# Optimization experiments

Hardware: AMD Instinct MI355X
Metric: run time of the kernel (lower is better)

## Reference

```python
import jax, jax.numpy as jnp
import numpy as np

B, T, C, H = 8, 1024, 1024, 16
D = C // H
EPS = 1e-5

def _ln(x, g, b):
    mu = jnp.mean(x, axis=-1, keepdims=True)
    var = jnp.var(x, axis=-1, keepdims=True)
    return (x - mu) * jax.lax.rsqrt(var + EPS) * g + b

def _build_mask(cond_mask, cond_len, token_len):
    # Vectorized form of the per-batch Python-loop mask in the torch module.
    counts = jnp.sum(cond_mask, axis=-1)            # [B] number of valid cond tokens
    rows = jnp.arange(T)
    cols = jnp.arange(T)
    # all rows may attend to the first counts[i] (cond) columns
    m_cond = cols[None, None, :] < counts[:, None, None]          # [B,1,T]
    m_cond = jnp.broadcast_to(m_cond, (B, T, T))
    # block-causal tiled pattern on rows/cols >= cond_len:
    # value = (col - cond_len) % token_len <= (row - cond_len) % token_len
    pattern = ((cols[None, :] - cond_len) % token_len) <= ((rows[:, None] - cond_len) % token_len)
    m_block = (rows[:, None] >= cond_len) & (cols[None, :] >= cond_len) & pattern  # [T,T]
    # cols >= cond_len: overwritten by block pattern (rows < cond_len stay 0 there)
    mask = jnp.where(cols[None, None, :] < cond_len, m_cond, m_block[None, :, :])
    return mask[:, None, :, :]                      # [B,1,T,T] bool

def _attn(x, Wq, bq, Wk, bk, Wv, bv, Wp, bp, cond_mask, cond_len, token_len):
    q = (x @ Wq + bq).reshape(B, T, H, D).transpose(0, 2, 1, 3)  # [B,H,T,D]
    k = (x @ Wk + bk).reshape(B, T, H, D).transpose(0, 2, 1, 3)
    v = (x @ Wv + bv).reshape(B, T, H, D).transpose(0, 2, 1, 3)
    att = jnp.einsum('bhqd,bhkd->bhqk', q, k) * (1.0 / np.sqrt(D))
    mask = _build_mask(cond_mask, cond_len, token_len)
    att = jnp.where(mask, att, -jnp.inf)
    att = jax.nn.softmax(att, axis=-1)
    y = jnp.einsum('bhqk,bhkd->bhqd', att, v)
    y = y.transpose(0, 2, 1, 3).reshape(B, T, C)
    return y @ Wp + bp

def setup_inputs() -> dict:
    key = jax.random.key(0)
    ks = jax.random.split(key, 16)
    cond_len, token_len = 256, 768
    s = 1.0 / np.sqrt(C)
    counts = jax.random.randint(ks[0], (B,), 1, cond_len + 1)
    cond_mask = (jnp.arange(T)[None, :] < counts[:, None]).astype(jnp.int32)
    return {
        'x': jax.random.normal(ks[1], (B, T, C), jnp.float32),
        'ln1_g': jnp.ones((C,), jnp.float32), 'ln1_b': jnp.zeros((C,), jnp.float32),
        'Wq': jax.random.normal(ks[2], (C, C), jnp.float32) * s, 'bq': jnp.zeros((C,), jnp.float32),
        'Wk': jax.random.normal(ks[3], (C, C), jnp.float32) * s, 'bk': jnp.zeros((C,), jnp.float32),
        'Wv': jax.random.normal(ks[4], (C, C), jnp.float32) * s, 'bv': jnp.zeros((C,), jnp.float32),
        'Wp': jax.random.normal(ks[5], (C, C), jnp.float32) * s, 'bp': jnp.zeros((C,), jnp.float32),
        'ln2_g': jnp.ones((C,), jnp.float32), 'ln2_b': jnp.zeros((C,), jnp.float32),
        'W1': jax.random.normal(ks[6], (C, 4 * C), jnp.float32) * s, 'b1': jnp.zeros((4 * C,), jnp.float32),
        'W2': jax.random.normal(ks[7], (4 * C, C), jnp.float32) * (0.5 * s), 'b2': jnp.zeros((C,), jnp.float32),
        'cond_mask': cond_mask,
        'cond_len': cond_len,
        'token_len': token_len,
    }

def reference(x, ln1_g, ln1_b, Wq, bq, Wk, bk, Wv, bv, Wp, bp, ln2_g, ln2_b, W1, b1, W2, b2, cond_mask, cond_len, token_len):
    x = x + _attn(_ln(x, ln1_g, ln1_b), Wq, bq, Wk, bk, Wv, bv, Wp, bp, cond_mask, cond_len, token_len)
    h = _ln(x, ln2_g, ln2_b)
    x = x + (jax.nn.gelu(h @ W1 + b1, approximate=False) @ W2 + b2)
    return x
```

## Files before the change

### kernel.cpp

```cpp
#include <hip/hip_runtime.h>
#include <hip/hip_bf16.h>
#include <cstdint>
#include <cstddef>

typedef __attribute__((ext_vector_type(8))) short short8;
typedef __attribute__((ext_vector_type(4))) float f32x4;
typedef __attribute__((ext_vector_type(4))) unsigned short us4;

#define MFMA_BF16(a, b, c) __builtin_amdgcn_mfma_f32_16x16x32_bf16((a), (b), (c), 0, 0, 0)
#define VMCNT(n) asm volatile("s_waitcnt vmcnt(" #n ")" ::: "memory")

__device__ __forceinline__ unsigned short f2bf(float f) {
  unsigned int u = __float_as_uint(f);
  u += 0x7FFFu + ((u >> 16) & 1u);
  return (unsigned short)(u >> 16);
}

__device__ __forceinline__ float gelu_fast(float v) {
  const float u = v * (0.79788456f + 0.03567741f * v * v);
  const float e = exp2f(u * 2.88539008f);
  return v - v * __builtin_amdgcn_rcpf(e + 1.0f);
}

typedef const void __attribute__((address_space(1)))* as1_cvp;
typedef void __attribute__((address_space(3)))* as3_vp;
__device__ __forceinline__ void gll16(const short* g, short* l) {
#if defined(__HIP_DEVICE_COMPILE__)
  __builtin_amdgcn_global_load_lds((as1_cvp)g, (as3_vp)l, 16, 0, 0);
#else
  (void)g; (void)l;
#endif
}

__global__ void count_kernel(const int* __restrict__ cm, int* __restrict__ counts) {
  __shared__ int sd[256];
  const int b = blockIdx.x, t = threadIdx.x;
  int s = 0;
  for (int i = t; i < 1024; i += 256) s += cm[b * 1024 + i];
  sd[t] = s; __syncthreads();
  for (int k = 128; k > 0; k >>= 1) { if (t < k) sd[t] += sd[t + k]; __syncthreads(); }
  if (t == 0) counts[b] = sd[0];
}

__global__ void pack_bias_kernel(const float* __restrict__ bq, const float* __restrict__ bk,
                                 const float* __restrict__ bv, float* __restrict__ dst) {
  int i = blockIdx.x * 256 + threadIdx.x;
  dst[i] = (i < 1024) ? bq[i] : (i < 2048 ? bk[i - 1024] : bv[i - 2048]);
}

__global__ void transpose_kernel(const float* __restrict__ src, unsigned short* __restrict__ dst,
                                 int R, int C) {
  __shared__ float tile[32][33];
  const int c0 = blockIdx.x * 32, r0 = blockIdx.y * 32;
  const int tx = threadIdx.x, ty = threadIdx.y;
  #pragma unroll
  for (int i = ty; i < 32; i += 8)
    tile[i][tx] = src[(size_t)(r0 + i) * C + (c0 + tx)];
  __syncthreads();
  #pragma unroll
  for (int i = ty; i < 32; i += 8)
    dst[(size_t)(c0 + i) * R + (r0 + tx)] = f2bf(tile[tx][i]);
}

__global__ void vtrans_kernel(const short* __restrict__ qkv, short* __restrict__ vtr) {
  __shared__ short tile[32][33];
  const int bh = blockIdx.z;
  const int t0 = blockIdx.x * 32, d0 = blockIdx.y * 32;
  const int b = bh >> 4, h = bh & 15;
  const int tx = threadIdx.x, ty = threadIdx.y;
  const short* src = qkv + (size_t)b * 1024 * 3072 + 2048 + h * 64;
  #pragma unroll
  for (int i = ty; i < 32; i += 8)
    tile[i][tx] = src[(size_t)(t0 + i) * 3072 + d0 + tx];
  __syncthreads();
  short* dst = vtr + (size_t)bh * 65536;
  #pragma unroll
  for (int i = ty; i < 32; i += 8)
    dst[(d0 + i) * 1024 + t0 + tx] = tile[tx][i];
}

__global__ __launch_bounds__(64) void kvpack_kernel(
    const short* __restrict__ qkv, const short* __restrict__ vtr,
    short* __restrict__ kp, short* __restrict__ vp) {
  const int blk = blockIdx.x;
  const int bh = blk >> 5, ti = blk & 31;
  const int b = bh >> 4, h = bh & 15;
  const int l = threadIdx.x & 63;
  const int lq = l & 15, g = l >> 4;
  const int kv0 = ti * 32;
  const int permrow = 8 * (lq >> 2) + (lq & 3);
  const short* ka = qkv + (size_t)b * 1024 * 3072 + h * 64
                    + (size_t)(kv0 + permrow) * 3072 + 1024 + 8 * g;
  short* kd = kp + (size_t)blk * 2048 + l * 8;
  *(short8*)(kd)        = *(const short8*)ka;
  *(short8*)(kd + 512)  = *(const short8*)(ka + 32);
  *(short8*)(kd + 1024) = *(const short8*)(ka + 4 * 3072);
  *(short8*)(kd + 1536) = *(const short8*)(ka + 4 * 3072 + 32);
  const short* vb = vtr + (size_t)bh * 65536;
  short* vd = vp + (size_t)blk * 2048 + l * 8;
  #pragma unroll
  for (int dc = 0; dc < 4; ++dc)
    *(short8*)(vd + dc * 512) =
        *(const short8*)(vb + (16 * dc + lq) * 1024 + kv0 + 8 * g);
}

__global__ __launch_bounds__(256) void ln_kernel(const float* __restrict__ in,
                                                 const float* __restrict__ gw,
                                                 const float* __restrict__ bw,
                                                 unsigned short* __restrict__ out) {
  const int row = blockIdx.x, t = threadIdx.x;
  const float4 v = ((const float4*)(in + (size_t)row * 1024))[t];
  float s = v.x + v.y + v.z + v.w;
  float ss = v.x * v.x + v.y * v.y + v.z * v.z + v.w * v.w;
  #pragma unroll
  for (int o = 32; o >= 1; o >>= 1) { s += __shfl_down(s, o, 64); ss += __shfl_down(ss, o, 64); }
  __shared__ float red[8];
  if ((t & 63) == 0) { red[t >> 6] = s; red[4 + (t >> 6)] = ss; }
  __syncthreads();
  const float S  = red[0] + red[1] + red[2] + red[3];
  const float SS = red[4] + red[5] + red[6] + red[7];
  const float mu = S * (1.0f / 1024.0f);
  const float var = SS * (1.0f / 1024.0f) - mu * mu;
  const float rs = rsqrtf(var + 1e-5f);
  const int c = t * 4;
  const float4 g4 = ((const float4*)gw)[t];
  const float4 b4 = ((const float4*)bw)[t];
  us4 o4;
  o4[0] = f2bf((v.x - mu) * rs * g4.x + b4.x);
  o4[1] = f2bf((v.y - mu) * rs * g4.y + b4.y);
  o4[2] = f2bf((v.z - mu) * rs * g4.z + b4.z);
  o4[3] = f2bf((v.w - mu) * rs * g4.w + b4.w);
  *(us4*)(out + (size_t)row * 1024 + c) = o4;
}

template <int EPI>
__global__ __launch_bounds__(256, 2) void gemm128_kernel(
    const short* __restrict__ A, const short* __restrict__ BT,
    const float* __restrict__ bias, int N, int K, int gm,
    unsigned short* __restrict__ outb, float* __restrict__ outf,
    const float* __restrict__ res) {
  __shared__ alignas(16) short lds[36864];
  const int t = threadIdx.x;
  const int l = t & 63, w = t >> 6;
  const int lq = l & 15, g = l >> 4;
  const int wc = w;
  const int cpx = (int)gridDim.x >> 3;
  const int wid = ((int)blockIdx.x & 7) * cpx + ((int)blockIdx.x >> 3);
  const int bm = (wid % gm) * 128, bn = (wid / gm) * 256;
  const int NT = K >> 5;

  const int csw = ((t & 3) ^ ((t >> 3) & 3)) * 8;
  const int sr = t >> 2;

  const f32x4 z4 = {0.f, 0.f, 0.f, 0.f};
  f32x4 acc[8][4];
  #pragma unroll
  for (int i = 0; i < 8; i++)
    #pragma unroll
    for (int j = 0; j < 4; j++) acc[i][j] = z4;

  auto stageA = [&](int buf, int k0) {
    const short* src = A + (size_t)(bm + sr) * K + k0 + csw;
    short* dst = lds + buf * 12288 + t * 8;
    gll16(src, dst);
    gll16(src + (size_t)64 * K, dst + 2048);
  };
  auto stageB = [&](int buf, int k0) {
    const short* src = BT + (size_t)(bn + sr) * K + k0 + csw;
    short* dst = lds + buf * 12288 + 4096 + t * 8;
    gll16(src, dst);
    gll16(src + (size_t)64 * K,  dst + 2048);
    gll16(src + (size_t)128 * K, dst + 4096);
    gll16(src + (size_t)192 * K, dst + 6144);
  };
  const int swu = (g ^ ((lq >> 1) & 3)) * 8;
  auto rdA = [&](int buf, int mi) {
    const int ra = mi * 16 + lq;
    return *(const short8*)(lds + buf * 12288 + ra * 32 + swu);
  };
  auto rdB = [&](int buf, int ni) {
    const int rb = wc * 64 + ni * 16 + lq;
    return *(const short8*)(lds + buf * 12288 + 4096 + rb * 32 + swu);
  };

  stageA(0, 0);  stageB(0, 0);
  stageA(1, 32); stageB(1, 32);
  VMCNT(6);
  __builtin_amdgcn_s_barrier();

  int cur = 0;
  for (int v = 0; v < NT; ++v) {
    const int nx1 = (cur == 2) ? 0 : cur + 1;
    const int nx2 = (nx1 == 2) ? 0 : nx1 + 1;
    short8 a[8], b[4];
    #pragma unroll
    for (int mi = 0; mi < 8; ++mi) a[mi] = rdA(cur, mi);
    #pragma unroll
    for (int ni = 0; ni < 4; ++ni) b[ni] = rdB(cur, ni);
    if (v + 2 < NT) {
      stageA(nx2, (v + 2) * 32); stageB(nx2, (v + 2) * 32);
      VMCNT(6);
    } else {
      VMCNT(0);
    }
    __builtin_amdgcn_s_barrier();
    __builtin_amdgcn_s_setprio(1);
    #pragma unroll
    for (int mi = 0; mi < 8; ++mi)
      #pragma unroll
      for (int ni = 0; ni < 4; ++ni)
        acc[mi][ni] = MFMA_BF16(a[mi], b[ni], acc[mi][ni]);
    __builtin_amdgcn_s_setprio(0);
    cur = nx1;
  }

  if (EPI == 2) {
    #pragma unroll
    for (int mi = 0; mi < 8; ++mi) {
      #pragma unroll
      for (int ni = 0; ni < 4; ++ni) {
        const int col = bn + wc * 64 + ni * 16 + lq;
        const float bv = bias[col];
        #pragma unroll
        for (int r = 0; r < 4; ++r) {
          const int row = bm + mi * 16 + 4 * g + r;
          const size_t idx = (size_t)row * N + col;
          outf[idx] = acc[mi][ni][r] + bv + res[idx];
        }
      }
    }
    return;
  }

  __syncthreads();
  const float qscale = (EPI == 3 && bn < 1024) ? 0.125f * 1.44269504088896f : 1.0f;
  unsigned short* eb = (unsigned short*)lds;
  #pragma unroll
  for (int mi = 0; mi < 8; ++mi) {
    #pragma unroll
    for (int ni = 0; ni < 4; ++ni) {
      const int col = wc * 64 + ni * 16 + lq;
      const float bv = bias[bn + col];
      #pragma unroll
      for (int r = 0; r < 4; ++r) {
        const int row = mi * 16 + 4 * g + r;
        float vv = acc[mi][ni][r] + bv;
        if (EPI == 1) vv = gelu_fast(vv);
        if (EPI == 3) vv *= qscale;
        eb[row * 256 + col] = f2bf(vv);
      }
    }
  }
  __syncthreads();
  #pragma unroll
  for (int it = 0; it < 16; ++it) {
    const int unit = it * 256 + t;
    const int row = unit >> 5, c8 = unit & 31;
    const short8 vv = *(const short8*)(lds + unit * 8);
    *(short8*)((short*)outb + (size_t)(bm + row) * N + bn + c8 * 8) = vv;
  }
}

__global__ __launch_bounds__(256) void attn_kernel(
    const short* __restrict__ qkv, const short* __restrict__ kp,
    const short* __restrict__ vp, unsigned short* __restrict__ y,
    const int* __restrict__ counts) {
  const int blk = blockIdx.x;
  const int slot = blk >> 3;
  const int pb = slot & 7;
  const int bh = ((slot >> 3) << 3) | (blk & 7);
  const int b = bh >> 4, h = bh & 15;
  const int w = threadIdx.x >> 6, l = threadIdx.x & 63;
  const int p = pb + 8 * w;
  const int lq = l & 15, g = l >> 4;
  const int qb0 = p * 16, qb1 = (63 - p) * 16;
  const int count = counts[b];

  const short* base  = qkv + (size_t)b * 1024 * 3072 + h * 64;
  const short* kbase = kp + (size_t)bh * 65536 + l * 8;
  const short* vbase = vp + (size_t)bh * 65536 + l * 8;

  short8 qf[2][2];
  {
    const short* qr0 = base + (size_t)(qb0 + lq) * 3072 + 8 * g;
    const short* qr1 = base + (size_t)(qb1 + lq) * 3072 + 8 * g;
    qf[0][0] = *(const short8*)qr0; qf[0][1] = *(const short8*)(qr0 + 32);
    qf[1][0] = *(const short8*)qr1; qf[1][1] = *(const short8*)(qr1 + 32);
  }

  const f32x4 z4 = {0.f, 0.f, 0.f, 0.f};
  f32x4 oacc[2][4];
  #pragma unroll
  for (int grp = 0; grp < 2; ++grp)
    #pragma unroll
    for (int dc = 0; dc < 4; ++dc) oacc[grp][dc] = z4;
  float mrun[2] = {-1e30f, -1e30f};
  float lrun[2] = {0.f, 0.f};
  const int ncond = min((count + 31) >> 5, 8);
  const int ncausal = (qb1 + 16 - 256 + 31) >> 5;
  const int nt = ncond + ncausal;
  auto kv_of = [&](int i) { return i < ncond ? i * 32 : 256 + (i - ncond) * 32; };

  auto loadt = [&](int kv0, short8 (&kr)[4], short8 (&vr)[4]) {
    const short* kpp = kbase + (size_t)(kv0 >> 5) * 2048;
    kr[0] = *(const short8*)kpp;
    kr[1] = *(const short8*)(kpp + 512);
    kr[2] = *(const short8*)(kpp + 1024);
    kr[3] = *(const short8*)(kpp + 1536);
    const short* vpp = vbase + (size_t)(kv0 >> 5) * 2048;
    #pragma unroll
    for (int dc = 0; dc < 4; ++dc)
      vr[dc] = *(const short8*)(vpp + dc * 512);
  };

  auto compute = [&](int i, const short8 (&kr)[4], const short8 (&vr)[4]) {
    const int kv0 = kv_of(i);
    const bool isCond = (i < ncond);
    #pragma unroll
    for (int grp = 0; grp < 2; ++grp) {
      const int qb = grp ? qb1 : qb0;
      if (!isCond && kv0 >= qb + 16) continue;
      const bool needMask = isCond ? (kv0 + 32 > count) : (kv0 + 31 > qb);
      f32x4 sA = z4, sB = z4;
      __builtin_amdgcn_s_setprio(1);
      sA = MFMA_BF16(kr[0], qf[grp][0], sA);
      sA = MFMA_BF16(kr[1], qf[grp][1], sA);
      sB = MFMA_BF16(kr[2], qf[grp][0], sB);
      sB = MFMA_BF16(kr[3], qf[grp][1], sB);
      __builtin_amdgcn_s_setprio(0);
      const int q = qb + lq;
      float mx = -1e30f;
      if (needMask) {
        #pragma unroll
        for (int r = 0; r < 4; ++r) {
          const int colA = kv0 + 8 * g + r, colB = colA + 4;
          const bool okA = isCond ? (colA < count) : (colA <= q);
          const bool okB = isCond ? (colB < count) : (colB <= q);
          const float vA = okA ? sA[r] : -1e30f;
          const float vB = okB ? sB[r] : -1e30f;
          sA[r] = vA; sB[r] = vB;
          mx = fmaxf(fmaxf(vA, vB), mx);
        }
      } else {
        #pragma unroll
        for (int r = 0; r < 4; ++r)
          mx = fmaxf(fmaxf(sA[r], sB[r]), mx);
      }
      mx = fmaxf(mx, __shfl_xor(mx, 16, 64));
      mx = fmaxf(mx, __shfl_xor(mx, 32, 64));
      float m = mrun[grp];
      if (!__all(mx <= m + 8.0f)) {
        const float mn = fmaxf(m, mx);
        const float sf = exp2f(m - mn);
        lrun[grp] *= sf;
        #pragma unroll
        for (int dc = 0; dc < 4; ++dc)
          #pragma unroll
          for (int r = 0; r < 4; ++r) oacc[grp][dc][r] *= sf;
        mrun[grp] = mn; m = mn;
      }
      float ps = 0.f;
      #pragma unroll
      for (int r = 0; r < 4; ++r) {
        const float aa = exp2f(sA[r] - m);
        const float c2 = exp2f(sB[r] - m);
        sA[r] = aa; sB[r] = c2; ps += aa + c2;
      }
      lrun[grp] += ps;
      union { short8 s8; __hip_bfloat162 h2[4]; } pu;
      pu.h2[0] = __float22bfloat162_rn(float2{sA[0], sA[1]});
      pu.h2[1] = __float22bfloat162_rn(float2{sA[2], sA[3]});
      pu.h2[2] = __float22bfloat162_rn(float2{sB[0], sB[1]});
      pu.h2[3] = __float22bfloat162_rn(float2{sB[2], sB[3]});
      __builtin_amdgcn_s_setprio(1);
      #pragma unroll
      for (int dc = 0; dc < 4; ++dc)
        oacc[grp][dc] = MFMA_BF16(vr[dc], pu.s8, oacc[grp][dc]);
      __builtin_amdgcn_s_setprio(0);
    }
  };

  short8 kb0[4], vb0[4], kb1[4], vb1[4];
  loadt(kv_of(0), kb0, vb0);
  for (int i = 0; i < nt; i += 2) {
    if (i + 1 < nt) loadt(kv_of(i + 1), kb1, vb1);
    compute(i, kb0, vb0);
    if (i + 1 >= nt) break;
    if (i + 2 < nt) loadt(kv_of(i + 2), kb0, vb0);
    compute(i + 1, kb1, vb1);
  }

  #pragma unroll
  for (int grp = 0; grp < 2; ++grp) {
    float ls = lrun[grp];
    ls += __shfl_xor(ls, 16, 64);
    ls += __shfl_xor(ls, 32, 64);
    const float inv = 1.0f / ls;
    const int qb = grp ? qb1 : qb0;
    unsigned short* yr = y + (size_t)(b * 1024 + qb + lq) * 1024 + h * 64;
    #pragma unroll
    for (int dc = 0; dc < 4; ++dc)
      #pragma unroll
      for (int r = 0; r < 4; ++r)
        yr[16 * dc + 4 * g + r] = f2bf(oacc[grp][dc][r] * inv);
  }
}

extern "C" void kernel_launch(void* const* d_in, const int* in_sizes, int n_in,
                              void* d_out, int out_size, void* d_ws, size_t ws_size,
                              hipStream_t stream) {
  (void)in_sizes; (void)n_in; (void)out_size; (void)ws_size;
  const float* x     = (const float*)d_in[0];
  const float* ln1_g = (const float*)d_in[1];
  const float* ln1_b = (const float*)d_in[2];
  const float* Wq    = (const float*)d_in[3];
  const float* bq    = (const float*)d_in[4];
  const float* Wk    = (const float*)d_in[5];
  const float* bk    = (const float*)d_in[6];
  const float* Wv    = (const float*)d_in[7];
  const float* bv    = (const float*)d_in[8];
  const float* Wp    = (const float*)d_in[9];
  const float* bp    = (const float*)d_in[10];
  const float* ln2_g = (const float*)d_in[11];
  const float* ln2_b = (const float*)d_in[12];
  const float* W1    = (const float*)d_in[13];
  const float* b1    = (const float*)d_in[14];
  const float* W2    = (const float*)d_in[15];
  const float* b2    = (const float*)d_in[16];
  const int* cond_mask = (const int*)d_in[17];

  char* ws = (char*)d_ws;
  const size_t MB = 1u << 20;
  short* xn    = (short*)(ws + 0);
  short* kpack = (short*)(ws + 0);
  short* qkv   = (short*)(ws + 16 * MB);
  short* act   = (short*)(ws + 0);
  unsigned short* yb = (unsigned short*)(ws + 64 * MB);
  short* vtr   = (short*)(ws + 80 * MB);
  float* x1    = (float*)(ws + 80 * MB);
  short* vpack = (short*)(ws + 112 * MB);
  short* hb    = (short*)(ws + 112 * MB);
  short* wqkvT = (short*)(ws + 128 * MB);
  short* wpT   = (short*)(ws + 134 * MB);
  short* w1T   = (short*)(ws + 136 * MB);
  short* w2T   = (short*)(ws + 144 * MB);
  float* bqkv  = (float*)(ws + 152 * MB);
  int* counts  = (int*)(ws + 152 * MB + 16384);

  const dim3 tb(32, 8);
  count_kernel<<<8, 256, 0, stream>>>(cond_mask, counts);
  pack_bias_kernel<<<12, 256, 0, stream>>>(bq, bk, bv, bqkv);
  transpose_kernel<<<dim3(32, 32), tb, 0, stream>>>(Wq, (unsigned short*)wqkvT, 1024, 1024);
  transpose_kernel<<<dim3(32, 32), tb, 0, stream>>>(Wk, (unsigned short*)(wqkvT + 1024 * 1024), 1024, 1024);
  transpose_kernel<<<dim3(32, 32), tb, 0, stream>>>(Wv, (unsigned short*)(wqkvT + 2 * 1024 * 1024), 1024, 1024);
  transpose_kernel<<<dim3(32, 32), tb, 0, stream>>>(Wp, (unsigned short*)wpT, 1024, 1024);
  transpose_kernel<<<dim3(128, 32), tb, 0, stream>>>(W1, (unsigned short*)w1T, 1024, 4096);
  transpose_kernel<<<dim3(32, 128), tb, 0, stream>>>(W2, (unsigned short*)w2T, 4096, 1024);
  ln_kernel<<<8192, 256, 0, stream>>>(x, ln1_g, ln1_b, (unsigned short*)xn);

  gemm128_kernel<3><<<768, 256, 0, stream>>>(xn, wqkvT, bqkv, 3072, 1024, 64,
                                             (unsigned short*)qkv, nullptr, nullptr);
  vtrans_kernel<<<dim3(32, 2, 128), tb, 0, stream>>>(qkv, vtr);
  kvpack_kernel<<<4096, 64, 0, stream>>>(qkv, vtr, kpack, vpack);
  attn_kernel<<<1024, 256, 0, stream>>>(qkv, kpack, vpack, yb, counts);
  gemm128_kernel<2><<<256, 256, 0, stream>>>((const short*)yb, wpT, bp, 1024, 1024, 64,
                                             nullptr, x1, x);
  ln_kernel<<<8192, 256, 0, stream>>>(x1, ln2_g, ln2_b, (unsigned short*)hb);
  gemm128_kernel<1><<<1024, 256, 0, stream>>>(hb, w1T, b1, 4096, 1024, 64,
                                              (unsigned short*)act, nullptr, nullptr);
  gemm128_kernel<2><<<256, 256, 0, stream>>>(act, w2T, b2, 1024, 4096, 64,
                                             nullptr, (float*)d_out, x1);
}
```

Measured before the change: 409.6 us.

## Split-K the FC2 GEMM into two slices with a separate reduction kernel

The final 4096-deep GEMM, previously launched with only 256 workgroups, now runs as two K-halves of 2048. This doubles the grid to 512 blocks so more of the CUs are busy. Each slice writes bf16 partial results, and a new elementwise kernel sums them and adds the bias and the residual in fp32. In exchange the kernel adds partial-buffer traffic and an extra launch, and the partials are rounded to bf16 before summation, which loses some precision.

```diff
diff --git a/kernel.cpp b/kernel.cpp
--- a/kernel.cpp
+++ b/kernel.cpp
@@ -133,19 +133,41 @@
   *(us4*)(out + (size_t)row * 1024 + c) = o4;
 }
 
+__global__ __launch_bounds__(256) void red_kernel(
+    const unsigned short* __restrict__ p0, const unsigned short* __restrict__ p1,
+    const float* __restrict__ bias, const float* __restrict__ res,
+    float* __restrict__ out) {
+  const int i = (blockIdx.x * 256 + threadIdx.x) * 4;
+  const us4 a = *(const us4*)(p0 + i);
+  const us4 b = *(const us4*)(p1 + i);
+  const float4 r = *(const float4*)(res + i);
+  const float4 bv = *(const float4*)(bias + (i & 1023));
+  float4 o;
+  o.x = __uint_as_float((unsigned)a[0] << 16) + __uint_as_float((unsigned)b[0] << 16) + bv.x + r.x;
+  o.y = __uint_as_float((unsigned)a[1] << 16) + __uint_as_float((unsigned)b[1] << 16) + bv.y + r.y;
+  o.z = __uint_as_float((unsigned)a[2] << 16) + __uint_as_float((unsigned)b[2] << 16) + bv.z + r.z;
+  o.w = __uint_as_float((unsigned)a[3] << 16) + __uint_as_float((unsigned)b[3] << 16) + bv.w + r.w;
+  *(float4*)(out + i) = o;
+}
+
 template <int EPI>
 __global__ __launch_bounds__(256, 2) void gemm128_kernel(
     const short* __restrict__ A, const short* __restrict__ BT,
-    const float* __restrict__ bias, int N, int K, int gm,
-    unsigned short* __restrict__ outb, float* __restrict__ outf,
-    const float* __restrict__ res) {
+    const float* __restrict__ bias, int N, int K, int kstr, int gm, int skoff,
+    unsigned short* __restrict__ outb, unsigned short* __restrict__ outb2,
+    float* __restrict__ outf, const float* __restrict__ res) {
   __shared__ alignas(16) short lds[36864];
   const int t = threadIdx.x;
   const int l = t & 63, w = t >> 6;
   const int lq = l & 15, g = l >> 4;
   const int wc = w;
   const int cpx = (int)gridDim.x >> 3;
-  const int wid = ((int)blockIdx.x & 7) * cpx + ((int)blockIdx.x >> 3);
+  int wid = ((int)blockIdx.x & 7) * cpx + ((int)blockIdx.x >> 3);
+  int slice = 0;
+  if (EPI == 4) { slice = wid >> 8; wid &= 255; }
+  const short* Ap = A + (size_t)slice * skoff;
+  const short* Bp = BT + (size_t)slice * skoff;
+  unsigned short* outp = (EPI == 4 && slice) ? outb2 : outb;
   const int bm = (wid % gm) * 128, bn = (wid / gm) * 256;
   const int NT = K >> 5;
 
@@ -160,18 +182,18 @@
     for (int j = 0; j < 4; j++) acc[i][j] = z4;
 
   auto stageA = [&](int buf, int k0) {
-    const short* src = A + (size_t)(bm + sr) * K + k0 + csw;
+    const short* src = Ap + (size_t)(bm + sr) * kstr + k0 + csw;
     short* dst = lds + buf * 12288 + t * 8;
     gll16(src, dst);
-    gll16(src + (size_t)64 * K, dst + 2048);
+    gll16(src + (size_t)64 * kstr, dst + 2048);
   };
   auto stageB = [&](int buf, int k0) {
-    const short* src = BT + (size_t)(bn + sr) * K + k0 + csw;
+    const short* src = Bp + (size_t)(bn + sr) * kstr + k0 + csw;
     short* dst = lds + buf * 12288 + 4096 + t * 8;
     gll16(src, dst);
-    gll16(src + (size_t)64 * K,  dst + 2048);
-    gll16(src + (size_t)128 * K, dst + 4096);
-    gll16(src + (size_t)192 * K, dst + 6144);
+    gll16(src + (size_t)64 * kstr,  dst + 2048);
+    gll16(src + (size_t)128 * kstr, dst + 4096);
+    gll16(src + (size_t)192 * kstr, dst + 6144);
   };
   const int swu = (g ^ ((lq >> 1) & 3)) * 8;
   auto rdA = [&](int buf, int mi) {
@@ -240,7 +262,7 @@
     #pragma unroll
     for (int ni = 0; ni < 4; ++ni) {
       const int col = wc * 64 + ni * 16 + lq;
-      const float bv = bias[bn + col];
+      const float bv = (EPI == 4) ? 0.f : bias[bn + col];
       #pragma unroll
       for (int r = 0; r < 4; ++r) {
         const int row = mi * 16 + 4 * g + r;
@@ -257,7 +279,7 @@
     const int unit = it * 256 + t;
     const int row = unit >> 5, c8 = unit & 31;
     const short8 vv = *(const short8*)(lds + unit * 8);
-    *(short8*)((short*)outb + (size_t)(bm + row) * N + bn + c8 * 8) = vv;
+    *(short8*)((short*)outp + (size_t)(bm + row) * N + bn + c8 * 8) = vv;
   }
 }
 
@@ -436,10 +458,12 @@
   short* qkv   = (short*)(ws + 16 * MB);
   short* act   = (short*)(ws + 0);
   unsigned short* yb = (unsigned short*)(ws + 64 * MB);
+  unsigned short* part0 = (unsigned short*)(ws + 64 * MB);
   short* vtr   = (short*)(ws + 80 * MB);
   float* x1    = (float*)(ws + 80 * MB);
   short* vpack = (short*)(ws + 112 * MB);
   short* hb    = (short*)(ws + 112 * MB);
+  unsigned short* part1 = (unsigned short*)(ws + 112 * MB);
   short* wqkvT = (short*)(ws + 128 * MB);
   short* wpT   = (short*)(ws + 134 * MB);
   short* w1T   = (short*)(ws + 136 * MB);
@@ -458,16 +482,17 @@
   transpose_kernel<<<dim3(32, 128), tb, 0, stream>>>(W2, (unsigned short*)w2T, 4096, 1024);
   ln_kernel<<<8192, 256, 0, stream>>>(x, ln1_g, ln1_b, (unsigned short*)xn);
 
-  gemm128_kernel<3><<<768, 256, 0, stream>>>(xn, wqkvT, bqkv, 3072, 1024, 64,
-                                             (unsigned short*)qkv, nullptr, nullptr);
+  gemm128_kernel<3><<<768, 256, 0, stream>>>(xn, wqkvT, bqkv, 3072, 1024, 1024, 64, 0,
+                                             (unsigned short*)qkv, nullptr, nullptr, nullptr);
   vtrans_kernel<<<dim3(32, 2, 128), tb, 0, stream>>>(qkv, vtr);
   kvpack_kernel<<<4096, 64, 0, stream>>>(qkv, vtr, kpack, vpack);
   attn_kernel<<<1024, 256, 0, stream>>>(qkv, kpack, vpack, yb, counts);
-  gemm128_kernel<2><<<256, 256, 0, stream>>>((const short*)yb, wpT, bp, 1024, 1024, 64,
-                                             nullptr, x1, x);
+  gemm128_kernel<2><<<256, 256, 0, stream>>>((const short*)yb, wpT, bp, 1024, 1024, 1024, 64, 0,
+                                             nullptr, nullptr, x1, x);
   ln_kernel<<<8192, 256, 0, stream>>>(x1, ln2_g, ln2_b, (unsigned short*)hb);
-  gemm128_kernel<1><<<1024, 256, 0, stream>>>(hb, w1T, b1, 4096, 1024, 64,
-                                              (unsigned short*)act, nullptr, nullptr);
-  gemm128_kernel<2><<<256, 256, 0, stream>>>(act, w2T, b2, 1024, 4096, 64,
-                                             nullptr, (float*)d_out, x1);
-}
+  gemm128_kernel<1><<<1024, 256, 0, stream>>>(hb, w1T, b1, 4096, 1024, 1024, 64, 0,
+                                              (unsigned short*)act, nullptr, nullptr, nullptr);
+  gemm128_kernel<4><<<512, 256, 0, stream>>>(act, w2T, nullptr, 1024, 2048, 4096, 64, 2048,
+                                             part0, part1, nullptr, nullptr);
+  red_kernel<<<8192, 256, 0, stream>>>(part0, part1, b2, x1, (float*)d_out);
+}
```

Result: no change. 408.8 us (-0.2%).
